# Optimization experiments

Measured on AMD Instinct MI355X. Metric: run time of the kernel, lower is better.

## Reference

```python
import jax, jax.numpy as jnp
import numpy as np

B = 2097152  # flattened batch of 3x3 rotation matrices

def setup_inputs() -> dict:
    key = jax.random.key(0)
    k1, k2 = jax.random.split(key)
    # scale by 0.1 so cos=(trace(m1 m2^T)-1)/2 stays strictly inside (-1,1)
    pred_rot = jax.random.normal(k1, (B, 3, 3), dtype=jnp.float32) * 0.1
    gt_rot = jax.random.normal(k2, (B, 3, 3), dtype=jnp.float32) * 0.1
    return {"pred_rot": pred_rot, "gt_rot": gt_rot}

def reference(pred_rot, gt_rot):
    m1 = pred_rot.reshape(-1, 3, 3)
    m2 = gt_rot.reshape(-1, 3, 3)
    # trace(m1 @ m2^T) == sum(m1 * m2) elementwise -> avoid the bmm
    cos = (jnp.einsum('bij,bij->b', m1, m2) - 1.0) * 0.5
    cos = jnp.clip(cos, -1.0, 1.0)  # min with +1, max with -1
    theta = jnp.arccos(cos)
    return jnp.mean(theta)  # reduction='mean'
```

## Files before the change

### kernel.cpp

```cpp
#include <hip/hip_runtime.h>
#include <math.h>


#define TPB 256
#define MPB 1024
#define F_PER_TILE 9216
#define F4_PER_TILE 2304

__global__ __launch_bounds__(TPB) void geo_kernel(
    const float* __restrict__ a, const float* __restrict__ b,
    float* __restrict__ out, float invM, int M)
{
    __shared__ float prod[F_PER_TILE];
    __shared__ float wsum[TPB / 64];

    const int tid = threadIdx.x;
    const long long tile_m0 = (long long)blockIdx.x * MPB;
    float sum = 0.0f;

    if (tile_m0 + MPB <= M) {
        const float4* __restrict__ a4 = (const float4*)(a + tile_m0 * 9);
        const float4* __restrict__ b4 = (const float4*)(b + tile_m0 * 9);
        #pragma unroll
        for (int k = 0; k < 9; ++k) {
            const int i = k * TPB + tid;
            float4 va = a4[i];
            float4 vb = b4[i];
            float4 p;
            p.x = va.x * vb.x; p.y = va.y * vb.y;
            p.z = va.z * vb.z; p.w = va.w * vb.w;
            ((float4*)prod)[i] = p;
        }
        __syncthreads();
        #pragma unroll
        for (int c = 0; c < 4; ++c) {
            const int base = 9 * (tid + 256 * c);
            float d = ((prod[base + 0] + prod[base + 1]) +
                       (prod[base + 2] + prod[base + 3])) +
                      ((prod[base + 4] + prod[base + 5]) +
                       (prod[base + 6] + prod[base + 7])) + prod[base + 8];
            float cv = fminf(1.0f, fmaxf(-1.0f, (d - 1.0f) * 0.5f));
            sum += acosf(cv);
        }
    } else {
        for (int c = 0; c < 4; ++c) {
            long long m = tile_m0 + tid + 256 * c;
            if (m < M) {
                float d = 0.0f;
                for (int j = 0; j < 9; ++j)
                    d = fmaf(a[m * 9 + j], b[m * 9 + j], d);
                float cv = fminf(1.0f, fmaxf(-1.0f, (d - 1.0f) * 0.5f));
                sum += acosf(cv);
            }
        }
    }

    #pragma unroll
    for (int off = 32; off > 0; off >>= 1)
        sum += __shfl_down(sum, off, 64);
    const int lane = tid & 63;
    const int wid  = tid >> 6;
    if (lane == 0) wsum[wid] = sum;
    __syncthreads();
    if (tid == 0) {
        float s = 0.0f;
        #pragma unroll
        for (int i = 0; i < TPB / 64; ++i) s += wsum[i];
        atomicAdd(out, s * invM);
    }
}

extern "C" void kernel_launch(void* const* d_in, const int* in_sizes, int n_in,
                              void* d_out, int out_size, void* d_ws, size_t ws_size,
                              hipStream_t stream) {
    const float* a = (const float*)d_in[0];
    const float* b = (const float*)d_in[1];
    float* out = (float*)d_out;

    const int n = in_sizes[0];
    const int M = n / 9;

    const int grid = (M + MPB - 1) / MPB;

    hipMemsetAsync(out, 0, (size_t)out_size * sizeof(float), stream);
    geo_kernel<<<grid, TPB, 0, stream>>>(a, b, out, 1.0f / (float)M, M);
}
```

Baseline: 167.0 us.

## Use persistent grid with register double-buffered tile prefetch

Replaces the one-tile-per-block launch with a fixed grid of 512 persistent blocks that loop over tiles, prefetching the next tile's 18 float4 loads into a second register set while the current tile is reduced through shared memory. This aims to hide global memory latency and cut the number of per-block atomics and block launches. It roughly doubles register pressure, which may reduce occupancy, and adds two barriers per tile. The tail is handled by a grid-stride loop.

Measured after the change: 166.7 us. Within noise of the previous version (-0.1%).

```diff
diff --git a/kernel.cpp b/kernel.cpp
--- a/kernel.cpp
+++ b/kernel.cpp
@@ -6,6 +6,49 @@
 #define MPB 1024
 #define F_PER_TILE 9216
 #define F4_PER_TILE 2304
+#define NBLOCKS 512
+
+#define DECL(S)                                                             \
+    float4 S##A0, S##A1, S##A2, S##A3, S##A4, S##A5, S##A6, S##A7, S##A8,   \
+           S##B0, S##B1, S##B2, S##B3, S##B4, S##B5, S##B6, S##B7, S##B8;
+
+#define LOADSET(S, t)                                                       \
+    {                                                                       \
+        const float4* __restrict__ pa = (const float4*)a + (t) * F4_PER_TILE + tid; \
+        const float4* __restrict__ pb = (const float4*)b + (t) * F4_PER_TILE + tid; \
+        S##A0 = pa[0];    S##A1 = pa[256];  S##A2 = pa[512];                \
+        S##A3 = pa[768];  S##A4 = pa[1024]; S##A5 = pa[1280];               \
+        S##A6 = pa[1536]; S##A7 = pa[1792]; S##A8 = pa[2048];               \
+        S##B0 = pb[0];    S##B1 = pb[256];  S##B2 = pb[512];                \
+        S##B3 = pb[768];  S##B4 = pb[1024]; S##B5 = pb[1280];               \
+        S##B6 = pb[1536]; S##B7 = pb[1792]; S##B8 = pb[2048];               \
+    }
+
+#define PK(S, k)                                                            \
+    {                                                                       \
+        float4 p;                                                           \
+        p.x = S##A##k.x * S##B##k.x; p.y = S##A##k.y * S##B##k.y;           \
+        p.z = S##A##k.z * S##B##k.z; p.w = S##A##k.w * S##B##k.w;           \
+        ((float4*)prod)[k * 256 + tid] = p;                                 \
+    }
+
+#define CONSUME(S)                                                          \
+    {                                                                       \
+        PK(S, 0) PK(S, 1) PK(S, 2) PK(S, 3) PK(S, 4)                        \
+        PK(S, 5) PK(S, 6) PK(S, 7) PK(S, 8)                                 \
+        __syncthreads();                                                    \
+        _Pragma("unroll")                                                   \
+        for (int c = 0; c < 4; ++c) {                                       \
+            const int bsx = 9 * (tid + 256 * c);                            \
+            float d = ((prod[bsx + 0] + prod[bsx + 1]) +                    \
+                       (prod[bsx + 2] + prod[bsx + 3])) +                   \
+                      ((prod[bsx + 4] + prod[bsx + 5]) +                    \
+                       (prod[bsx + 6] + prod[bsx + 7])) + prod[bsx + 8];    \
+            float cv = fminf(1.0f, fmaxf(-1.0f, (d - 1.0f) * 0.5f));        \
+            sum += acosf(cv);                                               \
+        }                                                                   \
+        __syncthreads();                                                    \
+    }
 
 __global__ __launch_bounds__(TPB) void geo_kernel(
     const float* __restrict__ a, const float* __restrict__ b,
@@ -15,43 +58,42 @@
     __shared__ float wsum[TPB / 64];
 
     const int tid = threadIdx.x;
-    const long long tile_m0 = (long long)blockIdx.x * MPB;
     float sum = 0.0f;
 
-    if (tile_m0 + MPB <= M) {
-        const float4* __restrict__ a4 = (const float4*)(a + tile_m0 * 9);
-        const float4* __restrict__ b4 = (const float4*)(b + tile_m0 * 9);
-        #pragma unroll
-        for (int k = 0; k < 9; ++k) {
-            const int i = k * TPB + tid;
-            float4 va = a4[i];
-            float4 vb = b4[i];
-            float4 p;
-            p.x = va.x * vb.x; p.y = va.y * vb.y;
-            p.z = va.z * vb.z; p.w = va.w * vb.w;
-            ((float4*)prod)[i] = p;
+    const long long ntf = (long long)M / MPB;
+    DECL(X) DECL(Y)
+
+    long long tile = blockIdx.x;
+    if (tile < ntf) {
+        LOADSET(X, tile)
+        int phase = 0;
+        for (;;) {
+            const long long next = tile + gridDim.x;
+            const bool more = (next < ntf);
+            if (phase == 0) {
+                if (more) LOADSET(Y, next)
+                asm volatile("" ::: "memory");
+                CONSUME(X)
+            } else {
+                if (more) LOADSET(X, next)
+                asm volatile("" ::: "memory");
+                CONSUME(Y)
+            }
+            if (!more) break;
+            tile = next;
+            phase ^= 1;
         }
-        __syncthreads();
-        #pragma unroll
-        for (int c = 0; c < 4; ++c) {
-            const int base = 9 * (tid + 256 * c);
-            float d = ((prod[base + 0] + prod[base + 1]) +
-                       (prod[base + 2] + prod[base + 3])) +
-                      ((prod[base + 4] + prod[base + 5]) +
-                       (prod[base + 6] + prod[base + 7])) + prod[base + 8];
+    }
+
+    {
+        const long long gid    = (long long)blockIdx.x * TPB + tid;
+        const long long stride = (long long)gridDim.x * TPB;
+        for (long long m = ntf * MPB + gid; m < M; m += stride) {
+            float d = 0.0f;
+            for (int j = 0; j < 9; ++j)
+                d = fmaf(a[m * 9 + j], b[m * 9 + j], d);
             float cv = fminf(1.0f, fmaxf(-1.0f, (d - 1.0f) * 0.5f));
             sum += acosf(cv);
-        }
-    } else {
-        for (int c = 0; c < 4; ++c) {
-            long long m = tile_m0 + tid + 256 * c;
-            if (m < M) {
-                float d = 0.0f;
-                for (int j = 0; j < 9; ++j)
-                    d = fmaf(a[m * 9 + j], b[m * 9 + j], d);
-                float cv = fminf(1.0f, fmaxf(-1.0f, (d - 1.0f) * 0.5f));
-                sum += acosf(cv);
-            }
         }
     }
 
@@ -80,8 +122,6 @@
     const int n = in_sizes[0];
     const int M = n / 9;
 
-    const int grid = (M + MPB - 1) / MPB;
-
     hipMemsetAsync(out, 0, (size_t)out_size * sizeof(float), stream);
-    geo_kernel<<<grid, TPB, 0, stream>>>(a, b, out, 1.0f / (float)M, M);
+    geo_kernel<<<NBLOCKS, TPB, 0, stream>>>(a, b, out, 1.0f / (float)M, M);
 }
```

## Switch to persistent per-wave tiles with wave barriers and fixed grid

Applied to the files above, without the earlier changes.

Each 64-lane wave now owns its own 256-matrix shared-memory slice and loops grid-stride over wave tiles, so only wave barriers are needed instead of block-wide syncthreads. The grid is fixed at 1024 blocks, which cuts the number of atomics from 2048 to 1024. All nine float4 loads per input are issued up front for memory-level parallelism. The tail is handled by a separate grid-stride scalar loop. The risk is less latency hiding if the fixed grid leaves the GPU under-occupied, and the wave barrier relies on lockstep execution within a wave for correctness.

Result: no change. 166.9 us (-0.1%).

```diff
diff --git a/kernel.cpp b/kernel.cpp
--- a/kernel.cpp
+++ b/kernel.cpp
@@ -3,69 +3,88 @@
 
 
 #define TPB 256
-#define MPB 1024
-#define F_PER_TILE 9216
-#define F4_PER_TILE 2304
+#define WPB 4
+#define MPW 256
+#define F_PER_WTILE 2304
+#define F4_PER_WTILE 576
+#define NBLOCKS 1024
 
-__global__ __launch_bounds__(TPB) void geo_kernel(
+__global__ __launch_bounds__(TPB, 4) void geo_kernel(
     const float* __restrict__ a, const float* __restrict__ b,
     float* __restrict__ out, float invM, int M)
 {
-    __shared__ float prod[F_PER_TILE];
-    __shared__ float wsum[TPB / 64];
+    __shared__ float prod[WPB * F_PER_WTILE];
+    __shared__ float wsum[WPB];
 
-    const int tid = threadIdx.x;
-    const long long tile_m0 = (long long)blockIdx.x * MPB;
+    const int tid  = threadIdx.x;
+    const int lane = tid & 63;
+    const int wid  = tid >> 6;
+    float* __restrict__ slice = prod + wid * F_PER_WTILE;
+    float4* __restrict__ slice4 = (float4*)slice;
+
+    const long long nwt = (long long)M / MPW;
+    const long long gw  = (long long)blockIdx.x * WPB + wid;
+    const long long nw  = (long long)gridDim.x * WPB;
+
     float sum = 0.0f;
 
-    if (tile_m0 + MPB <= M) {
-        const float4* __restrict__ a4 = (const float4*)(a + tile_m0 * 9);
-        const float4* __restrict__ b4 = (const float4*)(b + tile_m0 * 9);
-        #pragma unroll
-        for (int k = 0; k < 9; ++k) {
-            const int i = k * TPB + tid;
-            float4 va = a4[i];
-            float4 vb = b4[i];
-            float4 p;
-            p.x = va.x * vb.x; p.y = va.y * vb.y;
-            p.z = va.z * vb.z; p.w = va.w * vb.w;
-            ((float4*)prod)[i] = p;
-        }
-        __syncthreads();
+    for (long long t = gw; t < nwt; t += nw) {
+        const float4* __restrict__ pa = (const float4*)a + t * F4_PER_WTILE + lane;
+        const float4* __restrict__ pb = (const float4*)b + t * F4_PER_WTILE + lane;
+
+        float4 A0 = pa[0],   A1 = pa[64],  A2 = pa[128], A3 = pa[192],
+               A4 = pa[256], A5 = pa[320], A6 = pa[384], A7 = pa[448],
+               A8 = pa[512];
+        float4 B0 = pb[0],   B1 = pb[64],  B2 = pb[128], B3 = pb[192],
+               B4 = pb[256], B5 = pb[320], B6 = pb[384], B7 = pb[448],
+               B8 = pb[512];
+
+        #define PK(k)                                                       \
+            {                                                               \
+                float4 p;                                                   \
+                p.x = A##k.x * B##k.x; p.y = A##k.y * B##k.y;               \
+                p.z = A##k.z * B##k.z; p.w = A##k.w * B##k.w;               \
+                slice4[k * 64 + lane] = p;                                  \
+            }
+        PK(0) PK(1) PK(2) PK(3) PK(4) PK(5) PK(6) PK(7) PK(8)
+        #undef PK
+
+        __builtin_amdgcn_wave_barrier();
+
         #pragma unroll
         for (int c = 0; c < 4; ++c) {
-            const int base = 9 * (tid + 256 * c);
-            float d = ((prod[base + 0] + prod[base + 1]) +
-                       (prod[base + 2] + prod[base + 3])) +
-                      ((prod[base + 4] + prod[base + 5]) +
-                       (prod[base + 6] + prod[base + 7])) + prod[base + 8];
+            const int base = 9 * (lane + 64 * c);
+            float d = ((slice[base + 0] + slice[base + 1]) +
+                       (slice[base + 2] + slice[base + 3])) +
+                      ((slice[base + 4] + slice[base + 5]) +
+                       (slice[base + 6] + slice[base + 7])) + slice[base + 8];
             float cv = fminf(1.0f, fmaxf(-1.0f, (d - 1.0f) * 0.5f));
             sum += acosf(cv);
         }
-    } else {
-        for (int c = 0; c < 4; ++c) {
-            long long m = tile_m0 + tid + 256 * c;
-            if (m < M) {
-                float d = 0.0f;
-                for (int j = 0; j < 9; ++j)
-                    d = fmaf(a[m * 9 + j], b[m * 9 + j], d);
-                float cv = fminf(1.0f, fmaxf(-1.0f, (d - 1.0f) * 0.5f));
-                sum += acosf(cv);
-            }
+        __builtin_amdgcn_wave_barrier();
+    }
+
+    {
+        const long long gid    = (long long)blockIdx.x * TPB + tid;
+        const long long stride = (long long)gridDim.x * TPB;
+        for (long long m = nwt * MPW + gid; m < M; m += stride) {
+            float d = 0.0f;
+            for (int j = 0; j < 9; ++j)
+                d = fmaf(a[m * 9 + j], b[m * 9 + j], d);
+            float cv = fminf(1.0f, fmaxf(-1.0f, (d - 1.0f) * 0.5f));
+            sum += acosf(cv);
         }
     }
 
     #pragma unroll
     for (int off = 32; off > 0; off >>= 1)
         sum += __shfl_down(sum, off, 64);
-    const int lane = tid & 63;
-    const int wid  = tid >> 6;
     if (lane == 0) wsum[wid] = sum;
     __syncthreads();
     if (tid == 0) {
         float s = 0.0f;
         #pragma unroll
-        for (int i = 0; i < TPB / 64; ++i) s += wsum[i];
+        for (int i = 0; i < WPB; ++i) s += wsum[i];
         atomicAdd(out, s * invM);
     }
 }
@@ -80,8 +99,6 @@
     const int n = in_sizes[0];
     const int M = n / 9;
 
-    const int grid = (M + MPB - 1) / MPB;
-
     hipMemsetAsync(out, 0, (size_t)out_size * sizeof(float), stream);
-    geo_kernel<<<grid, TPB, 0, stream>>>(a, b, out, 1.0f / (float)M, M);
+    geo_kernel<<<NBLOCKS, TPB, 0, stream>>>(a, b, out, 1.0f / (float)M, M);
 }
```
